# Optimization experiments

Hardware: AMD Instinct MI355X
Metric: run time of the kernel (lower is better)

## Reference

```python
import jax, jax.numpy as jnp
import numpy as np
from jax import lax

B, C_IN, H_IN, W_IN = 32, 3, 128, 128
MID = 64
FINAL_HW = 13  # 128 ->conv 126 ->pool 62 ->conv 60 ->pool 29 ->conv 27 ->pool 13
EPS_SN = 1e-12
EPS_BN = 1e-5


def _norm(x):
    return x / jnp.maximum(jnp.linalg.norm(x), EPS_SN)


def setup_inputs() -> dict:
    key = jax.random.key(0)
    ks = jax.random.split(key, 10)
    x = jax.random.normal(ks[0], (B, C_IN, H_IN, W_IN), jnp.float32)
    w0 = jax.random.normal(ks[1], (MID, C_IN, 1, 1), jnp.float32) * 0.1
    w1 = jax.random.normal(ks[2], (MID, MID, 3, 3), jnp.float32) * 0.05
    w2 = jax.random.normal(ks[3], (MID, MID, 3, 3), jnp.float32) * 0.05
    w3 = jax.random.normal(ks[4], (MID, MID, 3, 3), jnp.float32) * 0.05
    gamma = jnp.ones((4, MID), jnp.float32)
    beta = jnp.zeros((4, MID), jnp.float32)
    # torch inits weight to zero / bias to identity; use small random weight so theta varies
    W_reg = jax.random.normal(ks[5], (6, MID * FINAL_HW * FINAL_HW), jnp.float32) * 0.01
    b_reg = jnp.array([1, 0, 0, 0, 1, 0], jnp.float32)
    u0 = _norm(jax.random.normal(ks[6], (2,), jnp.float32))
    v0 = _norm(jax.random.normal(ks[7], (3,), jnp.float32))
    return dict(x=x, w0=w0, w1=w1, w2=w2, w3=w3, gamma=gamma, beta=beta,
                W_reg=W_reg, b_reg=b_reg, u0=u0, v0=v0)


def reference(x, w0, w1, w2, w3, gamma, beta, W_reg, b_reg, u0, v0):
    conv = lambda h, w: lax.conv_general_dilated(
        h, w, (1, 1), 'VALID', dimension_numbers=('NCHW', 'OIHW', 'NCHW'))

    def bn_relu(h, g, b):  # BatchNorm2d in training mode (batch statistics)
        m = h.mean(axis=(0, 2, 3), keepdims=True)
        v = h.var(axis=(0, 2, 3), keepdims=True)
        return jax.nn.relu((h - m) / jnp.sqrt(v + EPS_BN) * g[None, :, None, None]
                           + b[None, :, None, None])

    def pool(h):  # MaxPool2d(kernel=3, stride=2)
        return lax.reduce_window(h, -jnp.inf, lax.max,
                                 (1, 1, 3, 3), (1, 1, 2, 2), 'VALID')

    # localization CNN
    h = bn_relu(conv(x, w0), gamma[0], beta[0])
    for i, wk in enumerate((w1, w2, w3)):
        h = bn_relu(pool(conv(h, wk)), gamma[i + 1], beta[i + 1])

    flat = h.reshape(h.shape[0], -1)
    theta = (flat @ W_reg.T + b_reg).reshape(-1, 2, 3)  # (B,2,3)

    # per-sample spectral normalization with u,v carried sequentially across batch
    def sample_step(carry, Wm):
        def power(c, _):
            u, v = c
            v = _norm(Wm.T @ u)
            u = _norm(Wm @ v)
            return (u, v), None
        (u, v), _ = lax.scan(power, carry, None, length=4)
        sigma = u @ (Wm @ v)
        return (u, v), Wm / sigma
    _, theta = lax.scan(sample_step, (u0, v0), theta)

    # affine_grid, align_corners=False
    N, Cc, Hh, Ww = x.shape
    xs = (2 * jnp.arange(Ww, dtype=x.dtype) + 1) / Ww - 1
    ys = (2 * jnp.arange(Hh, dtype=x.dtype) + 1) / Hh - 1
    base = jnp.stack([jnp.tile(xs[None, :], (Hh, 1)),
                      jnp.tile(ys[:, None], (1, Ww)),
                      jnp.ones((Hh, Ww), x.dtype)], axis=-1)  # (H,W,3)
    grid = jnp.einsum('nij,hwj->nhwi', theta, base)  # [...,0]=x, [...,1]=y

    # grid_sample: bilinear, padding_mode='reflection', align_corners=False
    ix = ((grid[..., 0] + 1) * Ww - 1) / 2
    iy = ((grid[..., 1] + 1) * Hh - 1) / 2

    def reflect(c, size):
        lo = -0.5
        span = jnp.asarray(size, c.dtype)
        r = jnp.mod(jnp.abs(c - lo), 2 * span)
        c = jnp.where(r > span, 2 * span - r, r) + lo
        return jnp.clip(c, 0.0, size - 1)

    ix = reflect(ix, Ww)
    iy = reflect(iy, Hh)
    x0 = jnp.floor(ix)
    y0 = jnp.floor(iy)
    wx = (ix - x0)[..., None]
    wy = (iy - y0)[..., None]
    x0i = jnp.clip(x0.astype(jnp.int32), 0, Ww - 1)
    x1i = jnp.clip(x0i + 1, 0, Ww - 1)
    y0i = jnp.clip(y0.astype(jnp.int32), 0, Hh - 1)
    y1i = jnp.clip(y0i + 1, 0, Hh - 1)
    bidx = jnp.arange(N)[:, None, None]
    g = lambda yy, xx: x[bidx, :, yy, xx]  # (N,H,W,C)
    out = (g(y0i, x0i) * (1 - wx) * (1 - wy) + g(y0i, x1i) * wx * (1 - wy)
           + g(y1i, x0i) * (1 - wx) * wy + g(y1i, x1i) * wx * wy)
    return out.transpose(0, 3, 1, 2)  # (N,C,H,W)
```

## Files before the change

kernel.cpp:

```cpp
#include <hip/hip_runtime.h>
#include <math.h>


typedef _Float16 half8_t __attribute__((ext_vector_type(8)));
typedef float f32x4 __attribute__((ext_vector_type(4)));

__device__ inline unsigned short f16bits(_Float16 h) {
  union { _Float16 h; unsigned short u; } cv; cv.h = h; return cv.u;
}

__global__ __launch_bounds__(256) void k_xstats(const float* __restrict__ x,
                                                float* __restrict__ xst) {
  int g0 = blockIdx.x * 256 + threadIdx.x;
  float a[9] = {0,0,0,0,0,0,0,0,0};
  for (int g = g0; g < 524288; g += 1024 * 256) {
    int b = g >> 14, p = g & 16383;
    const float* xb = x + (size_t)b * 49152 + p;
    float x0 = xb[0], x1 = xb[16384], x2 = xb[32768];
    a[0] += x0; a[1] += x1; a[2] += x2;
    a[3] += x0 * x0; a[4] += x0 * x1; a[5] += x0 * x2;
    a[6] += x1 * x1; a[7] += x1 * x2; a[8] += x2 * x2;
  }
  __shared__ float red[256];
  for (int k = 0; k < 9; ++k) {
    red[threadIdx.x] = a[k];
    __syncthreads();
    for (int s = 128; s > 0; s >>= 1) {
      if (threadIdx.x < s) red[threadIdx.x] += red[threadIdx.x + s];
      __syncthreads();
    }
    if (threadIdx.x == 0) atomicAdd(&xst[k], red[0]);
    __syncthreads();
  }
}

__global__ void k_bn0(const float* __restrict__ xst, const float* __restrict__ w0,
                      const float* __restrict__ gamma, const float* __restrict__ beta,
                      float* __restrict__ sb0) {
  int c = threadIdx.x;
  if (c >= 64) return;
  const float invN = 1.f / 524288.f;
  float mu0 = xst[0] * invN, mu1 = xst[1] * invN, mu2 = xst[2] * invN;
  float M00 = xst[3] * invN, M01 = xst[4] * invN, M02 = xst[5] * invN;
  float M11 = xst[6] * invN, M12 = xst[7] * invN, M22 = xst[8] * invN;
  float wa = w0[c * 3], wb = w0[c * 3 + 1], wc = w0[c * 3 + 2];
  float m  = wa * mu0 + wb * mu1 + wc * mu2;
  float e2 = wa * wa * M00 + wb * wb * M11 + wc * wc * M22
           + 2.f * (wa * wb * M01 + wa * wc * M02 + wb * wc * M12);
  float var = e2 - m * m;
  float sc = gamma[c] / sqrtf(var + 1e-5f);
  sb0[2 * c] = sc;
  sb0[2 * c + 1] = beta[c] - m * sc;
}

__global__ __launch_bounds__(256) void k_wprep(const float* __restrict__ w1,
                                               _Float16* __restrict__ Wp) {
  int i = blockIdx.x * 256 + threadIdx.x;
  if (i >= 36864) return;
  int s = i >> 12, rem = i & 4095;
  int ci = rem >> 6, co = rem & 63;
  float w = w1[(co * 64 + ci) * 9 + s];
  _Float16 hi = (_Float16)w;
  _Float16 lo = (_Float16)((w - (float)hi) * 2048.0f);
  int g = ci >> 3, e = ci & 7;
  Wp[(((size_t)(s * 2 + 0) * 8 + g) * 64 + co) * 8 + e] = hi;
  Wp[(((size_t)(s * 2 + 1) * 8 + g) * 64 + co) * 8 + e] = lo;
}

__global__ __launch_bounds__(256) void k_conv1_mfma(
    const float* __restrict__ x, const float* __restrict__ w0,
    const _Float16* __restrict__ Wp, const float* __restrict__ sb0,
    float* __restrict__ out) {
  __shared__ __align__(16) unsigned char smem[51488];
  float* x_lds = (float*)(smem + 47520);

  int bid = blockIdx.x;
  int cb = bid & 1, pr = (bid >> 1) % 62, b = (bid >> 1) / 62;
  int CB = cb * 62;
  int t = threadIdx.x;
  int lane = t & 63, wv = t >> 6;
  int cwv = wv * 16;
  int l15 = lane & 15, l4 = lane >> 4;

  for (int i = t; i < 990; i += 256) {
    int ch = i / 330, pos = i - ch * 330;
    int ir = pos / 66, ic = pos - ir * 66;
    x_lds[ch * 330 + pos] =
        x[((size_t)(b * 3 + ch) << 14) + (2 * pr + ir) * 128 + CB + ic];
  }

  f32x4 acc1[3][4], acc2[3][4];
  #pragma unroll
  for (int r = 0; r < 3; ++r)
    #pragma unroll
    for (int ct = 0; ct < 4; ++ct) {
      acc1[r][ct] = (f32x4)0.f;
      acc2[r][ct] = (f32x4)0.f;
    }

  int pair = t & 15;
  int posb = t >> 4;
  int LB = l15 * 144 + l4 * 16;

  for (int q = 0; q < 2; ++q) {
    int ci0 = q * 32 + 2 * pair, ci1 = ci0 + 1;
    float w00 = w0[ci0*3], w01 = w0[ci0*3+1], w02 = w0[ci0*3+2];
    float w10 = w0[ci1*3], w11 = w0[ci1*3+1], w12 = w0[ci1*3+2];
    float sc0 = sb0[2*ci0], bi0 = sb0[2*ci0+1];
    float sc1 = sb0[2*ci1], bi1 = sb0[2*ci1+1];
    __syncthreads();
    for (int pos = posb; pos < 330; pos += 16) {
      float x0 = x_lds[pos], x1 = x_lds[330 + pos], x2 = x_lds[660 + pos];
      float v0 = fmaxf(fmaf(fmaf(x2, w02, fmaf(x1, w01, x0 * w00)), sc0, bi0), 0.f);
      float v1 = fmaxf(fmaf(fmaf(x2, w12, fmaf(x1, w11, x0 * w10)), sc1, bi1), 0.f);
      _Float16 h0 = (_Float16)v0, h1 = (_Float16)v1;
      _Float16 g0 = (_Float16)((v0 - (float)h0) * 2048.f);
      _Float16 g1 = (_Float16)((v1 - (float)h1) * 2048.f);
      unsigned uh = f16bits(h0) | ((unsigned)f16bits(h1) << 16);
      unsigned ul = f16bits(g0) | ((unsigned)f16bits(g1) << 16);
      int base = pos * 144 + pair * 4;
      *(unsigned*)(smem + base) = uh;
      *(unsigned*)(smem + base + 64) = ul;
    }
    __syncthreads();

    #pragma unroll
    for (int s = 0; s < 9; ++s) {
      const int kh = s / 3, kw = s % 3;
      half8_t Ah[4], Al[4];
      #pragma unroll
      for (int ct = 0; ct < 4; ++ct) {
        Ah[ct] = *(const half8_t*)(Wp + ((size_t)((s*2+0)*8 + q*4 + l4) * 64 + ct*16 + l15) * 8);
        Al[ct] = *(const half8_t*)(Wp + ((size_t)((s*2+1)*8 + q*4 + l4) * 64 + ct*16 + l15) * 8);
      }
      #pragma unroll
      for (int r = 0; r < 3; ++r) {
        int rowoff = ((r + kh) * 66 + cwv + kw) * 144 + LB;
        half8_t Bh = *(const half8_t*)(smem + rowoff);
        half8_t Bl = *(const half8_t*)(smem + rowoff + 64);
        #pragma unroll
        for (int ct = 0; ct < 4; ++ct) {
          acc1[r][ct] = __builtin_amdgcn_mfma_f32_16x16x32_f16(Ah[ct], Bh, acc1[r][ct], 0, 0, 0);
          acc2[r][ct] = __builtin_amdgcn_mfma_f32_16x16x32_f16(Ah[ct], Bl, acc2[r][ct], 0, 0, 0);
          acc2[r][ct] = __builtin_amdgcn_mfma_f32_16x16x32_f16(Al[ct], Bh, acc2[r][ct], 0, 0, 0);
        }
      }
    }
  }

  __syncthreads();
  float* ctile = (float*)smem;
  #pragma unroll
  for (int r = 0; r < 3; ++r)
    #pragma unroll
    for (int ct = 0; ct < 4; ++ct)
      #pragma unroll
      for (int e = 0; e < 4; ++e) {
        int co = ct * 16 + l4 * 4 + e;
        ctile[(co * 3 + r) * 65 + cwv + l15] =
            acc1[r][ct][e] + acc2[r][ct][e] * (1.f / 2048.f);
      }
  __syncthreads();
  for (int i = t; i < 64 * 31; i += 256) {
    int co = i / 31, pcl = i - co * 31;
    float m = -INFINITY;
    #pragma unroll
    for (int dr = 0; dr < 3; ++dr)
      #pragma unroll
      for (int dc = 0; dc < 3; ++dc)
        m = fmaxf(m, ctile[(co * 3 + dr) * 65 + 2 * pcl + dc]);
    out[((size_t)(b * 64 + co) * 62 + pr) * 62 + cb * 31 + pcl] = m;
  }
}

template<int IN, int POOLW, int NH>
__global__ __launch_bounds__(256) void k_convpool_mfma(
    const float* __restrict__ in, const _Float16* __restrict__ Wp,
    const float* __restrict__ sb, float* __restrict__ out) {
  __shared__ __align__(16) unsigned char smem[25344];

  int bid = blockIdx.x;
  int h  = (NH == 2) ? (bid & 1) : 0;
  int pw = (NH == 2) ? (bid >> 1) : bid;
  int pr = pw % POOLW;
  int b  = pw / POOLW;
  int CB = h * 30;
  int t = threadIdx.x;
  int lane = t & 63, wv = t >> 6;
  int l15 = lane & 15, l4 = lane >> 4;
  int wc = wv & 1, wo = wv >> 1;

  f32x4 acc1[3][2], acc2[3][2];
  #pragma unroll
  for (int r = 0; r < 3; ++r)
    #pragma unroll
    for (int c = 0; c < 2; ++c) { acc1[r][c] = (f32x4)0.f; acc2[r][c] = (f32x4)0.f; }

  for (int q = 0; q < 2; ++q) {
    __syncthreads();
    for (int li = t; li < 5440; li += 256) {
      int ci = li / 170, pos = li - ci * 170;
      int ir = pos / 34, ic = pos - ir * 34;
      int gci = q * 32 + ci;
      int gc = CB + ic;
      float v = 0.f;
      if (gc < IN)
        v = fmaxf(fmaf(in[((size_t)(b * 64 + gci) * IN + 2 * pr + ir) * IN + gc],
                       sb[2 * gci], sb[2 * gci + 1]), 0.f);
      _Float16 hi = (_Float16)v;
      _Float16 lo = (_Float16)((v - (float)hi) * 2048.f);
      int base = pos * 144 + ci * 2;
      *(_Float16*)(smem + base) = hi;
      *(_Float16*)(smem + base + 64) = lo;
    }
    __syncthreads();
    #pragma unroll
    for (int s = 0; s < 9; ++s) {
      const int kh = s / 3, kw = s % 3;
      half8_t Ah[2], Al[2];
      #pragma unroll
      for (int cti = 0; cti < 2; ++cti) {
        int co = (wo * 2 + cti) * 16 + l15;
        Ah[cti] = *(const half8_t*)(Wp + ((size_t)((s*2+0)*8 + q*4 + l4) * 64 + co) * 8);
        Al[cti] = *(const half8_t*)(Wp + ((size_t)((s*2+1)*8 + q*4 + l4) * 64 + co) * 8);
      }
      #pragma unroll
      for (int r = 0; r < 3; ++r) {
        int rowoff = ((r + kh) * 34 + wc * 16 + l15 + kw) * 144 + l4 * 16;
        half8_t Bh = *(const half8_t*)(smem + rowoff);
        half8_t Bl = *(const half8_t*)(smem + rowoff + 64);
        #pragma unroll
        for (int cti = 0; cti < 2; ++cti) {
          acc1[r][cti] = __builtin_amdgcn_mfma_f32_16x16x32_f16(Ah[cti], Bh, acc1[r][cti], 0, 0, 0);
          acc2[r][cti] = __builtin_amdgcn_mfma_f32_16x16x32_f16(Ah[cti], Bl, acc2[r][cti], 0, 0, 0);
          acc2[r][cti] = __builtin_amdgcn_mfma_f32_16x16x32_f16(Al[cti], Bh, acc2[r][cti], 0, 0, 0);
        }
      }
    }
  }

  __syncthreads();
  float* ctile = (float*)smem;
  #pragma unroll
  for (int r = 0; r < 3; ++r)
    #pragma unroll
    for (int cti = 0; cti < 2; ++cti)
      #pragma unroll
      for (int e = 0; e < 4; ++e) {
        int co = (wo * 2 + cti) * 16 + l4 * 4 + e;
        ctile[(co * 3 + r) * 33 + wc * 16 + l15] =
            acc1[r][cti][e] + acc2[r][cti][e] * (1.f / 2048.f);
      }
  __syncthreads();
  constexpr int NPC = (NH == 1) ? POOLW : 15;
  int pc0 = h * 15;
  for (int i = t; i < 64 * NPC; i += 256) {
    int co = i / NPC, pcl = i - co * NPC;
    int pc = pc0 + pcl;
    if (pc >= POOLW) continue;
    float m = -INFINITY;
    #pragma unroll
    for (int dr = 0; dr < 3; ++dr)
      #pragma unroll
      for (int dc = 0; dc < 3; ++dc)
        m = fmaxf(m, ctile[(co * 3 + dr) * 33 + 2 * pcl + dc]);
    out[((size_t)(b * 64 + co) * POOLW + pr) * POOLW + pc] = m;
  }
}

__global__ __launch_bounds__(256) void k_stats(const float* __restrict__ h,
                                               float* __restrict__ st, int S) {
  int c = blockIdx.x & 63, b = blockIdx.x >> 6;
  const float* base = h + (size_t)(b * 64 + c) * S;
  float s = 0.f, s2 = 0.f;
  for (int i = threadIdx.x; i < S; i += 256) {
    float v = base[i]; s += v; s2 += v * v;
  }
  __shared__ float r1[256], r2[256];
  r1[threadIdx.x] = s; r2[threadIdx.x] = s2;
  __syncthreads();
  for (int str = 128; str > 0; str >>= 1) {
    if (threadIdx.x < str) {
      r1[threadIdx.x] += r1[threadIdx.x + str];
      r2[threadIdx.x] += r2[threadIdx.x + str];
    }
    __syncthreads();
  }
  if (threadIdx.x == 0) {
    atomicAdd(&st[2 * c],     r1[0]);
    atomicAdd(&st[2 * c + 1], r2[0]);
  }
}

__global__ void k_finalize(const float* __restrict__ st,
                           const float* __restrict__ gamma,
                           const float* __restrict__ beta,
                           float* __restrict__ sb, int layer, float invN) {
  int t = threadIdx.x;
  if (t >= 64) return;
  float m   = st[2 * t] * invN;
  float var = st[2 * t + 1] * invN - m * m;
  float sc  = gamma[layer * 64 + t] / sqrtf(var + 1e-5f);
  sb[2 * t]     = sc;
  sb[2 * t + 1] = beta[layer * 64 + t] - m * sc;
}

__global__ __launch_bounds__(256) void k_theta(const float* __restrict__ h3,
                                               const float* __restrict__ sb3,
                                               const float* __restrict__ Wreg,
                                               const float* __restrict__ breg,
                                               float* __restrict__ theta_raw) {
  int b = blockIdx.x, tid = threadIdx.x;
  float acc[6] = {0.f, 0.f, 0.f, 0.f, 0.f, 0.f};
  const float* hb = h3 + (size_t)b * 10816;
  for (int i = tid; i < 10816; i += 256) {
    int c = i / 169;
    float f = fmaxf(fmaf(hb[i], sb3[2 * c], sb3[2 * c + 1]), 0.f);
    #pragma unroll
    for (int j = 0; j < 6; ++j) acc[j] += f * Wreg[j * 10816 + i];
  }
  __shared__ float red[6][256];
  #pragma unroll
  for (int j = 0; j < 6; ++j) red[j][tid] = acc[j];
  __syncthreads();
  for (int s = 128; s > 0; s >>= 1) {
    if (tid < s) {
      #pragma unroll
      for (int j = 0; j < 6; ++j) red[j][tid] += red[j][tid + s];
    }
    __syncthreads();
  }
  if (tid < 6) theta_raw[b * 6 + tid] = red[tid][0] + breg[tid];
}

__global__ void k_spectral(const float* __restrict__ theta_raw,
                           const float* __restrict__ u0v,
                           const float* __restrict__ v0v,
                           float* __restrict__ theta) {
  if (threadIdx.x != 0 || blockIdx.x != 0) return;
  float ua = u0v[0], ub = u0v[1];
  float va = v0v[0], vb = v0v[1], vc = v0v[2];
  for (int n = 0; n < 32; ++n) {
    float W[6];
    #pragma unroll
    for (int k = 0; k < 6; ++k) W[k] = theta_raw[n * 6 + k];
    #pragma unroll
    for (int it = 0; it < 4; ++it) {
      float t0 = W[0]*ua + W[3]*ub;
      float t1 = W[1]*ua + W[4]*ub;
      float t2 = W[2]*ua + W[5]*ub;
      float nv = fmaxf(sqrtf(t0*t0 + t1*t1 + t2*t2), 1e-12f);
      va = t0/nv; vb = t1/nv; vc = t2/nv;
      float s0 = W[0]*va + W[1]*vb + W[2]*vc;
      float s1 = W[3]*va + W[4]*vb + W[5]*vc;
      float nu = fmaxf(sqrtf(s0*s0 + s1*s1), 1e-12f);
      ua = s0/nu; ub = s1/nu;
    }
    float s0 = W[0]*va + W[1]*vb + W[2]*vc;
    float s1 = W[3]*va + W[4]*vb + W[5]*vc;
    float sigma = ua*s0 + ub*s1;
    #pragma unroll
    for (int k = 0; k < 6; ++k) theta[n * 6 + k] = W[k] / sigma;
  }
}

__global__ __launch_bounds__(256) void k_sample(const float* __restrict__ x,
                                                const float* __restrict__ theta,
                                                float* __restrict__ out) {
  int idx = blockIdx.x * 256 + threadIdx.x;
  int b = idx >> 14, p = idx & 16383;
  int hh = p >> 7, ww = p & 127;
  const float* th = theta + b * 6;
  float xs = (2*ww + 1) * (1.f/128.f) - 1.f;
  float ys = (2*hh + 1) * (1.f/128.f) - 1.f;
  float gx = th[0]*xs + th[1]*ys + th[2];
  float gy = th[3]*xs + th[4]*ys + th[5];
  float ix = ((gx + 1.f) * 128.f - 1.f) * 0.5f;
  float iy = ((gy + 1.f) * 128.f - 1.f) * 0.5f;

  float r;
  r  = fmodf(fabsf(ix + 0.5f), 256.f);
  ix = ((r > 128.f) ? 256.f - r : r) - 0.5f;
  ix = fminf(fmaxf(ix, 0.f), 127.f);
  r  = fmodf(fabsf(iy + 0.5f), 256.f);
  iy = ((r > 128.f) ? 256.f - r : r) - 0.5f;
  iy = fminf(fmaxf(iy, 0.f), 127.f);

  float x0f = floorf(ix), y0f = floorf(iy);
  float wx = ix - x0f, wy = iy - y0f;
  int x0 = (int)x0f; x0 = min(max(x0, 0), 127); int x1 = min(x0 + 1, 127);
  int y0 = (int)y0f; y0 = min(max(y0, 0), 127); int y1 = min(y0 + 1, 127);
  float w00 = (1.f-wx)*(1.f-wy), w10 = wx*(1.f-wy);
  float w01 = (1.f-wx)*wy,       w11 = wx*wy;

  #pragma unroll
  for (int ch = 0; ch < 3; ++ch) {
    const float* xb = x + ((size_t)(b*3 + ch)) * 16384;
    float v = xb[y0*128 + x0]*w00 + xb[y0*128 + x1]*w10
            + xb[y1*128 + x0]*w01 + xb[y1*128 + x1]*w11;
    out[((size_t)(b*3 + ch)) * 16384 + p] = v;
  }
}

__global__ void k_zero(float* p, int n) {
  int i = blockIdx.x * 256 + threadIdx.x;
  if (i < n) p[i] = 0.f;
}

extern "C" void kernel_launch(void* const* d_in, const int* in_sizes, int n_in,
                              void* d_out, int out_size, void* d_ws, size_t ws_size,
                              hipStream_t stream) {
  const float* x     = (const float*)d_in[0];
  const float* w0    = (const float*)d_in[1];
  const float* w1    = (const float*)d_in[2];
  const float* w2    = (const float*)d_in[3];
  const float* w3    = (const float*)d_in[4];
  const float* gamma = (const float*)d_in[5];
  const float* beta  = (const float*)d_in[6];
  const float* Wreg  = (const float*)d_in[7];
  const float* breg  = (const float*)d_in[8];
  const float* u0v   = (const float*)d_in[9];
  const float* v0v   = (const float*)d_in[10];
  float* out = (float*)d_out;

  float* ws   = (float*)d_ws;
  float* h1   = ws;
  float* h2   = h1 + 7872512;
  float* h3   = h2 + 1722368;
  float* st   = h3 + 346112;
  float* xst  = st + 384;
  float* sb0  = xst + 16;
  float* sbL  = sb0 + 128;
  float* traw = sbL + 384;
  float* tfin = traw + 192;
  _Float16* Wp1 = (_Float16*)(tfin + 192);
  _Float16* Wp2 = Wp1 + 73728;
  _Float16* Wp3 = Wp2 + 73728;

  k_zero<<<2, 256, 0, stream>>>(st, 400);
  k_xstats<<<1024, 256, 0, stream>>>(x, xst);
  k_bn0<<<1, 64, 0, stream>>>(xst, w0, gamma, beta, sb0);
  k_wprep<<<144, 256, 0, stream>>>(w1, Wp1);
  k_wprep<<<144, 256, 0, stream>>>(w2, Wp2);
  k_wprep<<<144, 256, 0, stream>>>(w3, Wp3);

  k_conv1_mfma<<<32 * 62 * 2, 256, 0, stream>>>(x, w0, Wp1, sb0, h1);

  k_stats<<<2048, 256, 0, stream>>>(h1, st, 3844);
  k_finalize<<<1, 64, 0, stream>>>(st, gamma, beta, sbL, 1, 1.f / 123008.f);
  k_convpool_mfma<62, 29, 2><<<32 * 29 * 2, 256, 0, stream>>>(h1, Wp2, sbL, h2);

  k_stats<<<2048, 256, 0, stream>>>(h2, st + 128, 841);
  k_finalize<<<1, 64, 0, stream>>>(st + 128, gamma, beta, sbL + 128, 2, 1.f / 26912.f);
  k_convpool_mfma<29, 13, 1><<<32 * 13, 256, 0, stream>>>(h2, Wp3, sbL + 128, h3);

  k_stats<<<2048, 256, 0, stream>>>(h3, st + 256, 169);
  k_finalize<<<1, 64, 0, stream>>>(st + 256, gamma, beta, sbL + 256, 3, 1.f / 5408.f);

  k_theta<<<32, 256, 0, stream>>>(h3, sbL + 256, Wreg, breg, traw);
  k_spectral<<<1, 64, 0, stream>>>(traw, u0v, v0v, tfin);
  k_sample<<<2048, 256, 0, stream>>>(x, tfin, out);
}
```

Baseline: 587.8 us.

## Fuse prep and finalize kernels via last-block pattern; pad LDS stride to 140

Merges the three weight-prep launches and the zeroing kernel into one k_prep launch. The BN finalize steps are folded into the xstats and stats kernels using an atomic counter so the last block computes the scale and bias. This removes several tiny launches. Separately, the LDS row stride in the conv kernels changes from 144 to 140 bytes to alter bank mapping, which may break 16-byte alignment of the half8 loads. The counters are zeroed in k_prep alongside the stats buffer (404 floats covers st, xst and cnt).

```diff
diff --git a/kernel.cpp b/kernel.cpp
--- a/kernel.cpp
+++ b/kernel.cpp
@@ -9,8 +9,38 @@
   union { _Float16 h; unsigned short u; } cv; cv.h = h; return cv.u;
 }
 
+__global__ __launch_bounds__(256) void k_prep(const float* __restrict__ w1,
+                                              const float* __restrict__ w2,
+                                              const float* __restrict__ w3,
+                                              _Float16* __restrict__ Wp,
+                                              float* __restrict__ zb) {
+  int blk = blockIdx.x;
+  if (blk >= 432) {
+    int i = (blk - 432) * 256 + threadIdx.x;
+    if (i < 404) zb[i] = 0.f;
+    return;
+  }
+  int layer = blk / 144;
+  const float* w = (layer == 0) ? w1 : (layer == 1) ? w2 : w3;
+  _Float16* W = Wp + (size_t)layer * 73728;
+  int i = (blk % 144) * 256 + threadIdx.x;
+  int s = i >> 12, rem = i & 4095;
+  int ci = rem >> 6, co = rem & 63;
+  float wv = w[(co * 64 + ci) * 9 + s];
+  _Float16 hi = (_Float16)wv;
+  _Float16 lo = (_Float16)((wv - (float)hi) * 2048.0f);
+  int g = ci >> 3, e = ci & 7;
+  W[(((size_t)(s * 2 + 0) * 8 + g) * 64 + co) * 8 + e] = hi;
+  W[(((size_t)(s * 2 + 1) * 8 + g) * 64 + co) * 8 + e] = lo;
+}
+
 __global__ __launch_bounds__(256) void k_xstats(const float* __restrict__ x,
-                                                float* __restrict__ xst) {
+                                                float* __restrict__ xst,
+                                                unsigned* __restrict__ cnt,
+                                                const float* __restrict__ w0,
+                                                const float* __restrict__ gamma,
+                                                const float* __restrict__ beta,
+                                                float* __restrict__ sb0) {
   int g0 = blockIdx.x * 256 + threadIdx.x;
   float a[9] = {0,0,0,0,0,0,0,0,0};
   for (int g = g0; g < 524288; g += 1024 * 256) {
@@ -32,47 +62,39 @@
     if (threadIdx.x == 0) atomicAdd(&xst[k], red[0]);
     __syncthreads();
   }
-}
-
-__global__ void k_bn0(const float* __restrict__ xst, const float* __restrict__ w0,
-                      const float* __restrict__ gamma, const float* __restrict__ beta,
-                      float* __restrict__ sb0) {
+  __shared__ int lastf;
+  if (threadIdx.x == 0) {
+    __threadfence();
+    lastf = (atomicAdd(cnt, 1u) == (unsigned)(gridDim.x - 1));
+  }
+  __syncthreads();
+  if (!lastf) return;
+  __shared__ float xs[9];
+  if (threadIdx.x < 9) xs[threadIdx.x] = atomicAdd(&xst[threadIdx.x], 0.f);
+  __syncthreads();
   int c = threadIdx.x;
-  if (c >= 64) return;
-  const float invN = 1.f / 524288.f;
-  float mu0 = xst[0] * invN, mu1 = xst[1] * invN, mu2 = xst[2] * invN;
-  float M00 = xst[3] * invN, M01 = xst[4] * invN, M02 = xst[5] * invN;
-  float M11 = xst[6] * invN, M12 = xst[7] * invN, M22 = xst[8] * invN;
-  float wa = w0[c * 3], wb = w0[c * 3 + 1], wc = w0[c * 3 + 2];
-  float m  = wa * mu0 + wb * mu1 + wc * mu2;
-  float e2 = wa * wa * M00 + wb * wb * M11 + wc * wc * M22
-           + 2.f * (wa * wb * M01 + wa * wc * M02 + wb * wc * M12);
-  float var = e2 - m * m;
-  float sc = gamma[c] / sqrtf(var + 1e-5f);
-  sb0[2 * c] = sc;
-  sb0[2 * c + 1] = beta[c] - m * sc;
-}
-
-__global__ __launch_bounds__(256) void k_wprep(const float* __restrict__ w1,
-                                               _Float16* __restrict__ Wp) {
-  int i = blockIdx.x * 256 + threadIdx.x;
-  if (i >= 36864) return;
-  int s = i >> 12, rem = i & 4095;
-  int ci = rem >> 6, co = rem & 63;
-  float w = w1[(co * 64 + ci) * 9 + s];
-  _Float16 hi = (_Float16)w;
-  _Float16 lo = (_Float16)((w - (float)hi) * 2048.0f);
-  int g = ci >> 3, e = ci & 7;
-  Wp[(((size_t)(s * 2 + 0) * 8 + g) * 64 + co) * 8 + e] = hi;
-  Wp[(((size_t)(s * 2 + 1) * 8 + g) * 64 + co) * 8 + e] = lo;
+  if (c < 64) {
+    const float invN = 1.f / 524288.f;
+    float mu0 = xs[0]*invN, mu1 = xs[1]*invN, mu2 = xs[2]*invN;
+    float M00 = xs[3]*invN, M01 = xs[4]*invN, M02 = xs[5]*invN;
+    float M11 = xs[6]*invN, M12 = xs[7]*invN, M22 = xs[8]*invN;
+    float wa = w0[c*3], wb = w0[c*3+1], wc = w0[c*3+2];
+    float m  = wa*mu0 + wb*mu1 + wc*mu2;
+    float e2 = wa*wa*M00 + wb*wb*M11 + wc*wc*M22
+             + 2.f*(wa*wb*M01 + wa*wc*M02 + wb*wc*M12);
+    float var = e2 - m*m;
+    float sc = gamma[c] / sqrtf(var + 1e-5f);
+    sb0[2*c] = sc;
+    sb0[2*c+1] = beta[c] - m*sc;
+  }
 }
 
 __global__ __launch_bounds__(256) void k_conv1_mfma(
     const float* __restrict__ x, const float* __restrict__ w0,
     const _Float16* __restrict__ Wp, const float* __restrict__ sb0,
     float* __restrict__ out) {
-  __shared__ __align__(16) unsigned char smem[51488];
-  float* x_lds = (float*)(smem + 47520);
+  __shared__ __align__(16) unsigned char smem[50160];
+  float* x_lds = (float*)(smem + 46200);
 
   int bid = blockIdx.x;
   int cb = bid & 1, pr = (bid >> 1) % 62, b = (bid >> 1) / 62;
@@ -100,7 +122,7 @@
 
   int pair = t & 15;
   int posb = t >> 4;
-  int LB = l15 * 144 + l4 * 16;
+  int LB = l15 * 140 + l4 * 16;
 
   for (int q = 0; q < 2; ++q) {
     int ci0 = q * 32 + 2 * pair, ci1 = ci0 + 1;
@@ -118,7 +140,7 @@
       _Float16 g1 = (_Float16)((v1 - (float)h1) * 2048.f);
       unsigned uh = f16bits(h0) | ((unsigned)f16bits(h1) << 16);
       unsigned ul = f16bits(g0) | ((unsigned)f16bits(g1) << 16);
-      int base = pos * 144 + pair * 4;
+      int base = pos * 140 + pair * 4;
       *(unsigned*)(smem + base) = uh;
       *(unsigned*)(smem + base + 64) = ul;
     }
@@ -135,7 +157,7 @@
       }
       #pragma unroll
       for (int r = 0; r < 3; ++r) {
-        int rowoff = ((r + kh) * 66 + cwv + kw) * 144 + LB;
+        int rowoff = ((r + kh) * 66 + cwv + kw) * 140 + LB;
         half8_t Bh = *(const half8_t*)(smem + rowoff);
         half8_t Bl = *(const half8_t*)(smem + rowoff + 64);
         #pragma unroll
@@ -209,7 +231,7 @@
                        sb[2 * gci], sb[2 * gci + 1]), 0.f);
       _Float16 hi = (_Float16)v;
       _Float16 lo = (_Float16)((v - (float)hi) * 2048.f);
-      int base = pos * 144 + ci * 2;
+      int base = pos * 140 + ci * 2;
       *(_Float16*)(smem + base) = hi;
       *(_Float16*)(smem + base + 64) = lo;
     }
@@ -226,7 +248,7 @@
       }
       #pragma unroll
       for (int r = 0; r < 3; ++r) {
-        int rowoff = ((r + kh) * 34 + wc * 16 + l15 + kw) * 144 + l4 * 16;
+        int rowoff = ((r + kh) * 34 + wc * 16 + l15 + kw) * 140 + l4 * 16;
         half8_t Bh = *(const half8_t*)(smem + rowoff);
         half8_t Bl = *(const half8_t*)(smem + rowoff + 64);
         #pragma unroll
@@ -269,7 +291,12 @@
 }
 
 __global__ __launch_bounds__(256) void k_stats(const float* __restrict__ h,
-                                               float* __restrict__ st, int S) {
+                                               float* __restrict__ st, int S,
+                                               unsigned* __restrict__ cnt,
+                                               const float* __restrict__ gamma,
+                                               const float* __restrict__ beta,
+                                               float* __restrict__ sb,
+                                               int layer, float invN) {
   int c = blockIdx.x & 63, b = blockIdx.x >> 6;
   const float* base = h + (size_t)(b * 64 + c) * S;
   float s = 0.f, s2 = 0.f;
@@ -286,23 +313,25 @@
     }
     __syncthreads();
   }
+  __shared__ int lastf;
   if (threadIdx.x == 0) {
     atomicAdd(&st[2 * c],     r1[0]);
     atomicAdd(&st[2 * c + 1], r2[0]);
-  }
-}
-
-__global__ void k_finalize(const float* __restrict__ st,
-                           const float* __restrict__ gamma,
-                           const float* __restrict__ beta,
-                           float* __restrict__ sb, int layer, float invN) {
+    __threadfence();
+    lastf = (atomicAdd(cnt, 1u) == (unsigned)(gridDim.x - 1));
+  }
+  __syncthreads();
+  if (!lastf) return;
   int t = threadIdx.x;
-  if (t >= 64) return;
-  float m   = st[2 * t] * invN;
-  float var = st[2 * t + 1] * invN - m * m;
-  float sc  = gamma[layer * 64 + t] / sqrtf(var + 1e-5f);
-  sb[2 * t]     = sc;
-  sb[2 * t + 1] = beta[layer * 64 + t] - m * sc;
+  if (t < 64) {
+    float s1 = atomicAdd(&st[2 * t], 0.f);
+    float sq = atomicAdd(&st[2 * t + 1], 0.f);
+    float m   = s1 * invN;
+    float var = sq * invN - m * m;
+    float sc  = gamma[layer * 64 + t] / sqrtf(var + 1e-5f);
+    sb[2 * t]     = sc;
+    sb[2 * t + 1] = beta[layer * 64 + t] - m * sc;
+  }
 }
 
 __global__ __launch_bounds__(256) void k_theta(const float* __restrict__ h3,
@@ -400,11 +429,6 @@
             + xb[y1*128 + x0]*w01 + xb[y1*128 + x1]*w11;
     out[((size_t)(b*3 + ch)) * 16384 + p] = v;
   }
-}
-
-__global__ void k_zero(float* p, int n) {
-  int i = blockIdx.x * 256 + threadIdx.x;
-  if (i < n) p[i] = 0.f;
 }
 
 extern "C" void kernel_launch(void* const* d_in, const int* in_sizes, int n_in,
@@ -429,33 +453,24 @@
   float* h3   = h2 + 1722368;
   float* st   = h3 + 346112;
   float* xst  = st + 384;
-  float* sb0  = xst + 16;
+  unsigned* cnt = (unsigned*)(xst + 16);
+  float* sb0  = xst + 20;
   float* sbL  = sb0 + 128;
   float* traw = sbL + 384;
   float* tfin = traw + 192;
-  _Float16* Wp1 = (_Float16*)(tfin + 192);
-  _Float16* Wp2 = Wp1 + 73728;
-  _Float16* Wp3 = Wp2 + 73728;
-
-  k_zero<<<2, 256, 0, stream>>>(st, 400);
-  k_xstats<<<1024, 256, 0, stream>>>(x, xst);
-  k_bn0<<<1, 64, 0, stream>>>(xst, w0, gamma, beta, sb0);
-  k_wprep<<<144, 256, 0, stream>>>(w1, Wp1);
-  k_wprep<<<144, 256, 0, stream>>>(w2, Wp2);
-  k_wprep<<<144, 256, 0, stream>>>(w3, Wp3);
-
-  k_conv1_mfma<<<32 * 62 * 2, 256, 0, stream>>>(x, w0, Wp1, sb0, h1);
-
-  k_stats<<<2048, 256, 0, stream>>>(h1, st, 3844);
-  k_finalize<<<1, 64, 0, stream>>>(st, gamma, beta, sbL, 1, 1.f / 123008.f);
-  k_convpool_mfma<62, 29, 2><<<32 * 29 * 2, 256, 0, stream>>>(h1, Wp2, sbL, h2);
-
-  k_stats<<<2048, 256, 0, stream>>>(h2, st + 128, 841);
-  k_finalize<<<1, 64, 0, stream>>>(st + 128, gamma, beta, sbL + 128, 2, 1.f / 26912.f);
-  k_convpool_mfma<29, 13, 1><<<32 * 13, 256, 0, stream>>>(h2, Wp3, sbL + 128, h3);
-
-  k_stats<<<2048, 256, 0, stream>>>(h3, st + 256, 169);
-  k_finalize<<<1, 64, 0, stream>>>(st + 256, gamma, beta, sbL + 256, 3, 1.f / 5408.f);
+  _Float16* Wp = (_Float16*)(tfin + 192);
+
+  k_prep<<<434, 256, 0, stream>>>(w1, w2, w3, Wp, st);
+  k_xstats<<<1024, 256, 0, stream>>>(x, xst, cnt + 0, w0, gamma, beta, sb0);
+
+  k_conv1_mfma<<<32 * 62 * 2, 256, 0, stream>>>(x, w0, Wp, sb0, h1);
+  k_stats<<<2048, 256, 0, stream>>>(h1, st, 3844, cnt + 1, gamma, beta, sbL, 1, 1.f / 123008.f);
+
+  k_convpool_mfma<62, 29, 2><<<32 * 29 * 2, 256, 0, stream>>>(h1, Wp + 73728, sbL, h2);
+  k_stats<<<2048, 256, 0, stream>>>(h2, st + 128, 841, cnt + 2, gamma, beta, sbL + 128, 2, 1.f / 26912.f);
+
+  k_convpool_mfma<29, 13, 1><<<32 * 13, 256, 0, stream>>>(h2, Wp + 147456, sbL + 128, h3);
+  k_stats<<<2048, 256, 0, stream>>>(h3, st + 256, 169, cnt + 3, gamma, beta, sbL + 256, 3, 1.f / 5408.f);
 
   k_theta<<<32, 256, 0, stream>>>(h3, sbL + 256, Wreg, breg, traw);
   k_spectral<<<1, 64, 0, stream>>>(traw, u0v, v0v, tfin);
```

Result: slower. 765.3 us (+30.2%).
